# Optimization experiments

Hardware: AMD Instinct MI355X
Metric: run time of the kernel (lower is better)

## Reference

```python
import jax, jax.numpy as jnp
import numpy as np


def setup_inputs() -> dict:
    key = jax.random.key(0)
    k1, k2 = jax.random.split(key)
    L, O, N, D = 512, 512, 64, 512
    x = jax.random.normal(k1, (L, N, D), dtype=jnp.float32)
    upfold = jax.random.normal(k2, (O, N, D), dtype=jnp.float32)
    return {"x": x, "upfold": upfold}


def reference(x, upfold):
    # x: [L, N, D], upfold: [O, N, D]
    D = x.shape[-1]
    scale = 1.0 / jnp.sqrt(jnp.asarray(D, dtype=x.dtype))
    # affinities: [L, O, N]
    affinities = jnp.einsum('lnd,ond->lon', x, upfold) * scale
    # sigmoid-attention (no softmax normalization), centered at 0
    weights = jax.nn.sigmoid(affinities) - 0.5
    # features: [L, N, D]
    features = jnp.einsum('lon,ond->lnd', weights, upfold)
    return features
```

## Files before the change

kernel.cpp:

```cpp
#include <hip/hip_runtime.h>
#include <hip/hip_bf16.h>
#include <stdint.h>


typedef __attribute__((ext_vector_type(8))) short short8;
typedef __attribute__((ext_vector_type(4))) float f32x4;

__device__ __forceinline__ uint16_t f2bf(float f) {
    uint32_t u = __builtin_bit_cast(uint32_t, f);
    uint32_t r = u + 0x7FFFu + ((u >> 16) & 1u);
    return (uint16_t)(r >> 16);
}
__device__ __forceinline__ uint32_t cvt2(float a, float b) {
    return (uint32_t)f2bf(a) | ((uint32_t)f2bf(b) << 16);
}

__global__ __launch_bounds__(256) void kPrepUp(const float* __restrict__ up,
                                               uint16_t* __restrict__ ub,
                                               uint16_t* __restrict__ ut) {
    __shared__ float tile[64][65];
    int b = blockIdx.x;
    int n = b >> 6, r = b & 63;
    int o0 = (r >> 3) << 6, d0 = (r & 7) << 6;
    int tid = threadIdx.x;
    int i  = tid >> 2;
    int jq = (tid & 3) << 4;

    const float* src = up + ((size_t)(o0 + i) * 64 + n) * 512 + d0 + jq;
    float v[16];
    #pragma unroll
    for (int c = 0; c < 16; c += 4) {
        float4 q = *reinterpret_cast<const float4*>(src + c);
        v[c] = q.x; v[c+1] = q.y; v[c+2] = q.z; v[c+3] = q.w;
        tile[i][jq+c] = q.x; tile[i][jq+c+1] = q.y;
        tile[i][jq+c+2] = q.z; tile[i][jq+c+3] = q.w;
    }
    uint32_t pk[8];
    if (ub) {
        #pragma unroll
        for (int c = 0; c < 8; ++c) pk[c] = cvt2(v[2*c], v[2*c+1]);
        uint16_t* udst = ub + ((size_t)n * 512 + o0 + i) * 512 + d0 + jq;
        *reinterpret_cast<uint4*>(udst)     = *reinterpret_cast<const uint4*>(pk);
        *reinterpret_cast<uint4*>(udst + 8) = *reinterpret_cast<const uint4*>(pk + 4);
    }
    __syncthreads();
    #pragma unroll
    for (int c = 0; c < 8; ++c) pk[c] = cvt2(tile[jq + 2*c][i], tile[jq + 2*c + 1][i]);
    uint16_t* tdst = ut + ((size_t)n * 512 + d0 + i) * 512 + o0 + jq;
    *reinterpret_cast<uint4*>(tdst)     = *reinterpret_cast<const uint4*>(pk);
    *reinterpret_cast<uint4*>(tdst + 8) = *reinterpret_cast<const uint4*>(pk + 4);
}

__global__ __launch_bounds__(256) void kPrepX(const float* __restrict__ x,
                                              uint16_t* __restrict__ xb) {
    int b = blockIdx.x;
    int tid = threadIdx.x;
    int row = b * 4 + (tid >> 6);
    int l = row >> 6, n = row & 63;
    int d0 = (tid & 63) * 8;
    const float* src = x + (size_t)row * 512 + d0;
    float4 v0 = *reinterpret_cast<const float4*>(src);
    float4 v1 = *reinterpret_cast<const float4*>(src + 4);
    uint32_t pk[4] = {cvt2(v0.x, v0.y), cvt2(v0.z, v0.w),
                      cvt2(v1.x, v1.y), cvt2(v1.z, v1.w)};
    *reinterpret_cast<uint4*>(xb + ((size_t)n * 512 + l) * 512 + d0) =
        *reinterpret_cast<const uint4*>(pk);
}

template<int MODE>
__global__ __launch_bounds__(256) void kGemmT(const uint16_t* __restrict__ A,
                                              const uint16_t* __restrict__ B,
                                              void* __restrict__ outp) {
    __shared__ uint16_t As[128 * 64];
    __shared__ uint16_t Bs[128 * 64];
    int d = blockIdx.x;
    int n  = (d & 7) * 8 + (d >> 7);
    int t  = (d >> 3) & 15;
    int l0 = (t >> 2) << 7, c0 = (t & 3) << 7;
    int tid = threadIdx.x, lane = tid & 63, wid = tid >> 6;
    int wr = wid >> 1, wc = wid & 1;

    const char* An = (const char*)(A + (size_t)n * 262144);
    const char* Bn = (const char*)(B + (size_t)n * 262144);
    int rsub  = lane >> 3;
    int sbyte = ((lane & 7) ^ rsub) << 4;
    const char* gA = An + (size_t)(l0 + wid * 32 + rsub) * 1024 + sbyte;
    const char* gB = Bn + (size_t)(c0 + wid * 32 + rsub) * 1024 + sbyte;
    uint16_t* lA = As + wid * 32 * 64;
    uint16_t* lB = Bs + wid * 32 * 64;

    f32x4 acc[4][4];
    #pragma unroll
    for (int m = 0; m < 4; ++m)
        #pragma unroll
        for (int nf = 0; nf < 4; ++nf) acc[m][nf] = (f32x4)(0.f);

    for (int kt = 0; kt < 8; ++kt) {
        if (kt) __syncthreads();
        int gk = kt * 128;
        #pragma unroll
        for (int j = 0; j < 4; ++j) {
            __builtin_amdgcn_global_load_lds(
                (const __attribute__((address_space(1))) uint32_t*)(gA + gk + j * 8192),
                (__attribute__((address_space(3))) uint32_t*)(lA + j * 512), 16, 0, 0);
            __builtin_amdgcn_global_load_lds(
                (const __attribute__((address_space(1))) uint32_t*)(gB + gk + j * 8192),
                (__attribute__((address_space(3))) uint32_t*)(lB + j * 512), 16, 0, 0);
        }
        __syncthreads();
        #pragma unroll
        for (int kk = 0; kk < 2; ++kk) {
            short8 a[4], bb[4];
            int kbyte = kk * 64 + ((lane >> 4) * 16);
            #pragma unroll
            for (int m = 0; m < 4; ++m) {
                int row = wr * 64 + m * 16 + (lane & 15);
                int off = row * 128 + (kbyte ^ ((row & 7) << 4));
                a[m] = *reinterpret_cast<const short8*>((const char*)As + off);
            }
            #pragma unroll
            for (int nf = 0; nf < 4; ++nf) {
                int row = wc * 64 + nf * 16 + (lane & 15);
                int off = row * 128 + (kbyte ^ ((row & 7) << 4));
                bb[nf] = *reinterpret_cast<const short8*>((const char*)Bs + off);
            }
            #pragma unroll
            for (int m = 0; m < 4; ++m)
                #pragma unroll
                for (int nf = 0; nf < 4; ++nf)
                    acc[m][nf] = __builtin_amdgcn_mfma_f32_16x16x32_bf16(
                        a[m], bb[nf], acc[m][nf], 0, 0, 0);
        }
    }

    if constexpr (MODE == 1) {
        uint16_t* Wn = (uint16_t*)outp + (size_t)n * 262144;
        const float scale = 0.044194173824159216f;
        #pragma unroll
        for (int m = 0; m < 4; ++m) {
            int lrow0 = l0 + wr * 64 + m * 16 + ((lane >> 4) << 2);
            #pragma unroll
            for (int nf = 0; nf < 4; ++nf) {
                int ocol = c0 + wc * 64 + nf * 16 + (lane & 15);
                #pragma unroll
                for (int r = 0; r < 4; ++r) {
                    float aff = acc[m][nf][r] * scale;
                    float w = 1.f / (1.f + __expf(-aff)) - 0.5f;
                    Wn[(size_t)(lrow0 + r) * 512 + ocol] = f2bf(w);
                }
            }
        }
    } else {
        float* On = (float*)outp;
        #pragma unroll
        for (int m = 0; m < 4; ++m) {
            int lrow0 = l0 + wr * 64 + m * 16 + ((lane >> 4) << 2);
            #pragma unroll
            for (int nf = 0; nf < 4; ++nf) {
                int dcol = c0 + wc * 64 + nf * 16 + (lane & 15);
                #pragma unroll
                for (int r = 0; r < 4; ++r)
                    On[((size_t)(lrow0 + r) * 64 + n) * 512 + dcol] = acc[m][nf][r];
            }
        }
    }
}

__global__ __launch_bounds__(256) void kGemm1f32(const float* __restrict__ x,
                                                 const float* __restrict__ up,
                                                 uint16_t* __restrict__ W) {
    __shared__ uint16_t As[128 * 64];
    __shared__ uint16_t Bs[128 * 64];
    int b   = blockIdx.x;
    int n   = b >> 4;
    int t   = b & 15;
    int l0  = (t >> 2) << 7, o0 = (t & 3) << 7;
    int tid = threadIdx.x, lane = tid & 63, wid = tid >> 6;
    int wr = wid >> 1, wc = wid & 1;

    f32x4 acc[4][4];
    #pragma unroll
    for (int m = 0; m < 4; ++m)
        #pragma unroll
        for (int nf = 0; nf < 4; ++nf) acc[m][nf] = (f32x4)(0.f);

    int srow = tid >> 1;
    int kh   = (tid & 1) * 32;
    int swz  = (srow & 7) << 4;
    const float* aSrc = x  + ((size_t)(l0 + srow) * 64 + n) * 512 + kh;
    const float* bSrc = up + ((size_t)(o0 + srow) * 64 + n) * 512 + kh;

    for (int kt = 0; kt < 8; ++kt) {
        __syncthreads();
        const float* pA = aSrc + kt * 64;
        const float* pB = bSrc + kt * 64;
        #pragma unroll
        for (int c2 = 0; c2 < 4; ++c2) {
            float4 a0 = *reinterpret_cast<const float4*>(pA + c2 * 8);
            float4 a1 = *reinterpret_cast<const float4*>(pA + c2 * 8 + 4);
            float4 b0 = *reinterpret_cast<const float4*>(pB + c2 * 8);
            float4 b1 = *reinterpret_cast<const float4*>(pB + c2 * 8 + 4);
            uint32_t pa[4] = {cvt2(a0.x,a0.y), cvt2(a0.z,a0.w), cvt2(a1.x,a1.y), cvt2(a1.z,a1.w)};
            uint32_t pb[4] = {cvt2(b0.x,b0.y), cvt2(b0.z,b0.w), cvt2(b1.x,b1.y), cvt2(b1.z,b1.w)};
            int off = srow * 128 + (((kh * 2) + c2 * 16) ^ swz);
            *reinterpret_cast<uint4*>((char*)As + off) = *reinterpret_cast<const uint4*>(pa);
            *reinterpret_cast<uint4*>((char*)Bs + off) = *reinterpret_cast<const uint4*>(pb);
        }
        __syncthreads();
        #pragma unroll
        for (int kk = 0; kk < 2; ++kk) {
            short8 a[4], bf[4];
            int kbyte = kk * 64 + ((lane >> 4) * 16);
            #pragma unroll
            for (int m = 0; m < 4; ++m) {
                int row = wr * 64 + m * 16 + (lane & 15);
                int off = row * 128 + (kbyte ^ ((row & 7) << 4));
                a[m] = *reinterpret_cast<const short8*>((char*)As + off);
            }
            #pragma unroll
            for (int nf = 0; nf < 4; ++nf) {
                int row = wc * 64 + nf * 16 + (lane & 15);
                int off = row * 128 + (kbyte ^ ((row & 7) << 4));
                bf[nf] = *reinterpret_cast<const short8*>((char*)Bs + off);
            }
            #pragma unroll
            for (int m = 0; m < 4; ++m)
                #pragma unroll
                for (int nf = 0; nf < 4; ++nf)
                    acc[m][nf] = __builtin_amdgcn_mfma_f32_16x16x32_bf16(
                        a[m], bf[nf], acc[m][nf], 0, 0, 0);
        }
    }
    const float scale = 0.044194173824159216f;
    #pragma unroll
    for (int m = 0; m < 4; ++m) {
        int lrow0 = l0 + wr * 64 + m * 16 + ((lane >> 4) << 2);
        #pragma unroll
        for (int nf = 0; nf < 4; ++nf) {
            int ocol = o0 + wc * 64 + nf * 16 + (lane & 15);
            #pragma unroll
            for (int r = 0; r < 4; ++r) {
                float aff = acc[m][nf][r] * scale;
                float w = 1.f / (1.f + __expf(-aff)) - 0.5f;
                W[((size_t)n * 512 + (lrow0 + r)) * 512 + ocol] = f2bf(w);
            }
        }
    }
}

__global__ __launch_bounds__(256) void kNaive(const float* __restrict__ x,
                                              const float* __restrict__ up,
                                              float* __restrict__ out) {
    __shared__ float xr[512];
    __shared__ float w[512];
    int b = blockIdx.x;
    int l = b >> 6, n = b & 63;
    int tid = threadIdx.x;
    const float* xrow = x + ((size_t)l * 64 + n) * 512;
    xr[tid] = xrow[tid];
    xr[tid + 256] = xrow[tid + 256];
    __syncthreads();
    const float scale = 0.044194173824159216f;
    #pragma unroll
    for (int oo = 0; oo < 2; ++oo) {
        int o = tid + oo * 256;
        const float* ur = up + ((size_t)o * 64 + n) * 512;
        float s = 0.f;
        for (int dd = 0; dd < 512; ++dd) s += xr[dd] * ur[dd];
        w[o] = 1.f / (1.f + __expf(-s * scale)) - 0.5f;
    }
    __syncthreads();
    #pragma unroll
    for (int dd = 0; dd < 2; ++dd) {
        int d = tid + dd * 256;
        float f = 0.f;
        for (int o = 0; o < 512; ++o)
            f += w[o] * up[((size_t)o * 64 + n) * 512 + d];
        out[((size_t)l * 64 + n) * 512 + d] = f;
    }
}

extern "C" void kernel_launch(void* const* d_in, const int* in_sizes, int n_in,
                              void* d_out, int out_size, void* d_ws, size_t ws_size,
                              hipStream_t stream) {
    const float* x  = (const float*)d_in[0];
    const float* up = (const float*)d_in[1];
    float* out = (float*)d_out;

    const size_t MB32 = (size_t)64 * 512 * 512 * 2;
    if (ws_size >= 4 * MB32) {
        uint16_t* XB = (uint16_t*)d_ws;
        uint16_t* UB = XB + 16777216;
        uint16_t* UT = UB + 16777216;
        uint16_t* W  = UT + 16777216;
        kPrepUp<<<4096, 256, 0, stream>>>(up, UB, UT);
        kPrepX <<<8192, 256, 0, stream>>>(x, XB);
        kGemmT<1><<<1024, 256, 0, stream>>>(XB, UB, W);
        kGemmT<2><<<1024, 256, 0, stream>>>(W, UT, out);
    } else if (ws_size >= 2 * MB32) {
        uint16_t* UT = (uint16_t*)d_ws;
        uint16_t* W  = UT + 16777216;
        kPrepUp<<<4096, 256, 0, stream>>>(up, nullptr, UT);
        kGemm1f32<<<1024, 256, 0, stream>>>(x, up, W);
        kGemmT<2><<<1024, 256, 0, stream>>>(W, UT, out);
    } else {
        kNaive<<<512 * 64, 256, 0, stream>>>(x, up, out);
    }
}
```

Before: 119.4 us.

## Double-buffer LDS tiles in bf16 GEMM to overlap global loads with MFMA

Doubles the shared-memory A/B tiles and issues the next k-tile's global-to-LDS loads before computing on the current buffer, replacing the load/sync/compute serialization with a ping-pong pipeline. The aim is to hide global memory latency behind MFMA work. It doubles LDS use to 64 KB per block, which may lower occupancy. It also relies on explicit vmcnt waits plus raw s_barrier, with no lgkmcnt wait for the LDS reads before the buffer is overwritten.

```diff
diff --git a/kernel.cpp b/kernel.cpp
--- a/kernel.cpp
+++ b/kernel.cpp
@@ -71,8 +71,8 @@
 __global__ __launch_bounds__(256) void kGemmT(const uint16_t* __restrict__ A,
                                               const uint16_t* __restrict__ B,
                                               void* __restrict__ outp) {
-    __shared__ uint16_t As[128 * 64];
-    __shared__ uint16_t Bs[128 * 64];
+    __shared__ uint16_t As[2][8192];
+    __shared__ uint16_t Bs[2][8192];
     int d = blockIdx.x;
     int n  = (d & 7) * 8 + (d >> 7);
     int t  = (d >> 3) & 15;
@@ -86,8 +86,6 @@
     int sbyte = ((lane & 7) ^ rsub) << 4;
     const char* gA = An + (size_t)(l0 + wid * 32 + rsub) * 1024 + sbyte;
     const char* gB = Bn + (size_t)(c0 + wid * 32 + rsub) * 1024 + sbyte;
-    uint16_t* lA = As + wid * 32 * 64;
-    uint16_t* lB = Bs + wid * 32 * 64;
 
     f32x4 acc[4][4];
     #pragma unroll
@@ -95,19 +93,29 @@
         #pragma unroll
         for (int nf = 0; nf < 4; ++nf) acc[m][nf] = (f32x4)(0.f);
 
-    for (int kt = 0; kt < 8; ++kt) {
-        if (kt) __syncthreads();
-        int gk = kt * 128;
+    auto STAGE = [&](int buf, int kt) {
+        const char* pA = gA + kt * 128;
+        const char* pB = gB + kt * 128;
+        uint16_t* lA = &As[buf][wid * 2048];
+        uint16_t* lB = &Bs[buf][wid * 2048];
         #pragma unroll
         for (int j = 0; j < 4; ++j) {
             __builtin_amdgcn_global_load_lds(
-                (const __attribute__((address_space(1))) uint32_t*)(gA + gk + j * 8192),
+                (const __attribute__((address_space(1))) uint32_t*)(pA + j * 8192),
                 (__attribute__((address_space(3))) uint32_t*)(lA + j * 512), 16, 0, 0);
             __builtin_amdgcn_global_load_lds(
-                (const __attribute__((address_space(1))) uint32_t*)(gB + gk + j * 8192),
+                (const __attribute__((address_space(1))) uint32_t*)(pB + j * 8192),
                 (__attribute__((address_space(3))) uint32_t*)(lB + j * 512), 16, 0, 0);
         }
-        __syncthreads();
+    };
+
+    STAGE(0, 0);
+    asm volatile("s_waitcnt vmcnt(0)" ::: "memory");
+    __builtin_amdgcn_s_barrier();
+
+    int cur = 0;
+    for (int kt = 0; kt < 8; ++kt) {
+        if (kt < 7) STAGE(cur ^ 1, kt + 1);
         #pragma unroll
         for (int kk = 0; kk < 2; ++kk) {
             short8 a[4], bb[4];
@@ -116,13 +124,13 @@
             for (int m = 0; m < 4; ++m) {
                 int row = wr * 64 + m * 16 + (lane & 15);
                 int off = row * 128 + (kbyte ^ ((row & 7) << 4));
-                a[m] = *reinterpret_cast<const short8*>((const char*)As + off);
+                a[m] = *reinterpret_cast<const short8*>((const char*)As[cur] + off);
             }
             #pragma unroll
             for (int nf = 0; nf < 4; ++nf) {
                 int row = wc * 64 + nf * 16 + (lane & 15);
                 int off = row * 128 + (kbyte ^ ((row & 7) << 4));
-                bb[nf] = *reinterpret_cast<const short8*>((const char*)Bs + off);
+                bb[nf] = *reinterpret_cast<const short8*>((const char*)Bs[cur] + off);
             }
             #pragma unroll
             for (int m = 0; m < 4; ++m)
@@ -131,6 +139,11 @@
                     acc[m][nf] = __builtin_amdgcn_mfma_f32_16x16x32_bf16(
                         a[m], bb[nf], acc[m][nf], 0, 0, 0);
         }
+        if (kt < 7) {
+            asm volatile("s_waitcnt vmcnt(0)" ::: "memory");
+            __builtin_amdgcn_s_barrier();
+        }
+        cur ^= 1;
     }
 
     if constexpr (MODE == 1) {
```

Result: faster. 112.6 us (-5.7%).
